# Optimization experiments

Measured on AMD Instinct MI355X. Metric: run time of the kernel, lower is better.

The kernel has to match this reference:

```python
import jax, jax.numpy as jnp
import numpy as np

N, D, NUM_CLASSES = 8192, 128, 1000


def setup_inputs() -> dict:
    key = jax.random.key(0)
    ka, kb, kt = jax.random.split(key, 3)
    fa = jax.random.normal(ka, (N, D), dtype=jnp.float32)
    fb = jax.random.normal(kb, (N, D), dtype=jnp.float32)
    # L2-normalize as in standard contrastive setups (CLIP-style)
    fa = fa / jnp.linalg.norm(fa, axis=-1, keepdims=True)
    fb = fb / jnp.linalg.norm(fb, axis=-1, keepdims=True)
    targets = jax.random.randint(kt, (N,), 0, NUM_CLASSES, dtype=jnp.int64 if jax.config.jax_enable_x64 else jnp.int32)
    T = jnp.array([100.0], dtype=jnp.float32)  # logit scale
    return {
        "T": T,
        "local_features_a": fa,
        "local_features_b": fb,
        "global_targets": targets,
        "training": 1,
    }


def reference(T, local_features_a, local_features_b, global_targets, training):
    # world_size = 1: local features ARE the global features; the chunked
    # online-softmax reduction in the original is mathematically identical
    # to a stable logsumexp over the full logits row (max is detached, so
    # gradients also match).
    eq = (global_targets[:, None] == global_targets[None, :]).astype(jnp.float32)  # [N, N] positive mask
    target_sum = jnp.sum(eq, axis=-1)  # [N]

    def one_direction(fa, fb):
        logits = T * (fa @ fb.T)  # [N, N]
        weighted = -jnp.sum(eq * logits, axis=-1)            # sum of -logits over positives
        lse = jax.nn.logsumexp(logits, axis=-1)              # online-softmax global reduction
        per_row = weighted / target_sum + lse                # [N]
        return jnp.mean(per_row)

    loss_i = one_direction(local_features_a, local_features_b)
    loss_t = one_direction(local_features_b, local_features_a)
    return (loss_i + loss_t) / 2.0
```

## Files before the change

kernel.cpp:

```cpp
#include <hip/hip_runtime.h>
#include <hip/hip_bf16.h>

#define CN 8192
#define CD 128
#define NCLS 1000
#define MAXC 256

typedef __attribute__((ext_vector_type(8))) short bf16x8;
typedef __attribute__((ext_vector_type(4))) float f32x4;

#define WS_B_OFF     0x200000u
#define WS_CNT_OFF   0x400000u
#define WS_EXTRA_OFF 0x401000u
#define WS_ROWE_OFF  0x402000u
#define WS_COLE_OFF  0x40A000u
#define WS_BKT_OFF   0x412000u
#define WS_ROWP_OFF  0x490000u
#define WS_COLP_OFF  0x890000u
#define WS_FAST_BYTES 0xA90000u
#define WS_ZERO_BYTES 0x12000u

__device__ inline unsigned short f2bf(float f) {
    unsigned int u = __float_as_uint(f);
    return (unsigned short)((u + 0x7FFFu + ((u >> 16) & 1u)) >> 16);
}

__global__ void convert_kernel(const float* __restrict__ fa, const float* __restrict__ fb,
                               unsigned short* __restrict__ Abf, unsigned short* __restrict__ Bbf,
                               const int* __restrict__ tgt,
                               int* __restrict__ cnt, unsigned short* __restrict__ bucket) {
    int gid = blockIdx.x * 256 + threadIdx.x;
    int i = gid * 4;
    const float* src = blockIdx.y == 0 ? fa : fb;
    unsigned short* dst = blockIdx.y == 0 ? Abf : Bbf;
    float4 v = *reinterpret_cast<const float4*>(src + i);
    ushort4 o;
    o.x = f2bf(v.x); o.y = f2bf(v.y); o.z = f2bf(v.z); o.w = f2bf(v.w);
    *reinterpret_cast<ushort4*>(dst + i) = o;

    if (blockIdx.y == 0 && (gid & 31) == 0) {
        int row = gid >> 5;
        int t = tgt[row];
        int slot = atomicAdd(&cnt[t], 1);
        if (slot < MAXC) bucket[t * MAXC + slot] = (unsigned short)row;
    }
}

__global__ __launch_bounds__(64) void classsum_kernel(
    const float* __restrict__ Tptr,
    const float* __restrict__ fa, const float* __restrict__ fb,
    const int* __restrict__ cnt, const unsigned short* __restrict__ bucket,
    float* __restrict__ extra) {
    const int c = blockIdx.x;
    const int lane = threadIdx.x;
    const int n = cnt[c];
    const int m = n < MAXC ? n : MAXC;
    const float* src = lane < 32 ? fa : fb;
    const int d = (lane & 31) * 4;
    float ax = 0.f, ay = 0.f, az = 0.f, aw = 0.f;
    for (int s = 0; s < m; ++s) {
        int row = bucket[c * MAXC + s];
        float4 v = *reinterpret_cast<const float4*>(src + (size_t)row * CD + d);
        ax += v.x; ay += v.y; az += v.z; aw += v.w;
    }
    float bx_ = __shfl_xor(ax, 32), by_ = __shfl_xor(ay, 32);
    float bz_ = __shfl_xor(az, 32), bw_ = __shfl_xor(aw, 32);
    float p = ax * bx_ + ay * by_ + az * bz_ + aw * bw_;
    #pragma unroll
    for (int off = 1; off < 32; off <<= 1) p += __shfl_xor(p, off);
    if (lane == 0) extra[c] = n > 0 ? (-2.0f * Tptr[0] * p / (float)n) : 0.f;
}

__global__ __launch_bounds__(256) void tile_kernel(
    const float* __restrict__ Tptr,
    const unsigned short* __restrict__ Abf,
    const unsigned short* __restrict__ Bbf,
    float* __restrict__ rowE, float* __restrict__ colE,
    float* __restrict__ rowPart, float* __restrict__ colPart,
    int store_mode)
{
    __shared__ __align__(16) unsigned short sA[128 * 128];
    __shared__ __align__(16) unsigned short sB[64 * 128];
    __shared__ float colRed[4][64];

    const int tid  = threadIdx.x;
    const int brow = blockIdx.y * 128;
    const int bcol = blockIdx.x * 64;
    const float T   = Tptr[0];
    const float Tl2 = T * 1.44269504088896340736f;

    #pragma unroll
    for (int it = 0; it < 8; ++it) {
        int idx = it * 256 + tid;
        int r = idx >> 4, q = idx & 15;
        const unsigned short* src = Abf + (size_t)(brow + r) * CD + ((q ^ (r & 7)) * 8);
        __builtin_amdgcn_global_load_lds((const __attribute__((address_space(1))) void*)src,
                                         (__attribute__((address_space(3))) void*)&sA[idx * 8],
                                         16, 0, 0);
    }
    #pragma unroll
    for (int it = 0; it < 4; ++it) {
        int idx = it * 256 + tid;
        int r = idx >> 4, q = idx & 15;
        const unsigned short* src = Bbf + (size_t)(bcol + r) * CD + ((q ^ (r & 7)) * 8);
        __builtin_amdgcn_global_load_lds((const __attribute__((address_space(1))) void*)src,
                                         (__attribute__((address_space(3))) void*)&sB[idx * 8],
                                         16, 0, 0);
    }
    __syncthreads();

    const int lane = tid & 63;
    const int w    = tid >> 6;
    const int colg = lane & 15;
    const int rowg = lane >> 4;

    f32x4 acc[2][4];
    #pragma unroll
    for (int m = 0; m < 2; ++m)
        #pragma unroll
        for (int n = 0; n < 4; ++n)
            acc[m][n] = (f32x4){0.f, 0.f, 0.f, 0.f};

    #pragma unroll
    for (int kk = 0; kk < 4; ++kk) {
        bf16x8 af[2], bfr[4];
        #pragma unroll
        for (int m = 0; m < 2; ++m) {
            int r = w * 32 + m * 16 + colg;
            int slot = (kk * 4 + rowg) ^ (r & 7);
            af[m] = *reinterpret_cast<const bf16x8*>(&sA[r * 128 + slot * 8]);
        }
        #pragma unroll
        for (int n = 0; n < 4; ++n) {
            int r = n * 16 + colg;
            int slot = (kk * 4 + rowg) ^ (r & 7);
            bfr[n] = *reinterpret_cast<const bf16x8*>(&sB[r * 128 + slot * 8]);
        }
        #pragma unroll
        for (int m = 0; m < 2; ++m)
            #pragma unroll
            for (int n = 0; n < 4; ++n)
                acc[m][n] = __builtin_amdgcn_mfma_f32_16x16x32_bf16(af[m], bfr[n], acc[m][n], 0, 0, 0);
    }

    float rE[2][4] = {{0.f}};
    float cE[4] = {0.f, 0.f, 0.f, 0.f};
    #pragma unroll
    for (int m = 0; m < 2; ++m)
        #pragma unroll
        for (int n = 0; n < 4; ++n)
            #pragma unroll
            for (int j = 0; j < 4; ++j) {
                float e = exp2f(__builtin_fmaf(acc[m][n][j], Tl2, -Tl2));
                rE[m][j] += e;
                cE[n]    += e;
            }

    #pragma unroll
    for (int m = 0; m < 2; ++m)
        #pragma unroll
        for (int j = 0; j < 4; ++j) {
            float e = rE[m][j];
            #pragma unroll
            for (int off = 1; off < 16; off <<= 1) e += __shfl_xor(e, off);
            if (colg == 0) {
                int row = brow + w * 32 + m * 16 + rowg * 4 + j;
                if (store_mode) rowPart[(size_t)blockIdx.x * CN + row] = e;
                else            atomicAdd(&rowE[row], e);
            }
        }
    #pragma unroll
    for (int n = 0; n < 4; ++n) {
        float e = cE[n];
        e += __shfl_xor(e, 16);
        e += __shfl_xor(e, 32);
        if (rowg == 0) colRed[w][n * 16 + colg] = e;
    }
    __syncthreads();
    if (tid < 64) {
        float s = colRed[0][tid] + colRed[1][tid] + colRed[2][tid] + colRed[3][tid];
        if (store_mode) colPart[(size_t)blockIdx.y * CN + bcol + tid] = s;
        else            atomicAdd(&colE[bcol + tid], s);
    }
}

__global__ __launch_bounds__(256) void finalize_kernel(
    const float* __restrict__ Tptr,
    const float* __restrict__ rowE, const float* __restrict__ colE,
    const float* __restrict__ rowPart, const float* __restrict__ colPart,
    const float* __restrict__ extra,
    float* __restrict__ out, int store_mode)
{
    __shared__ float red[4];
    const int tid = threadIdx.x;
    int i = blockIdx.x * 256 + tid;
    const float T = Tptr[0];
    float v = 0.f;
    if (i < CN) {
        float se;
        if (store_mode) {
            se = 0.f;
            #pragma unroll 4
            for (int p = 0; p < 128; ++p) se += rowPart[(size_t)p * CN + i];
        } else se = rowE[i];
        v = T + logf(se);
    } else if (i < 2 * CN) {
        int c = i - CN;
        float se;
        if (store_mode) {
            se = 0.f;
            #pragma unroll 4
            for (int p = 0; p < 64; ++p) se += colPart[(size_t)p * CN + c];
        } else se = colE[c];
        v = T + logf(se);
    } else if (i < 2 * CN + NCLS) {
        v = extra[i - 2 * CN];
    }
    #pragma unroll
    for (int off = 1; off < 64; off <<= 1) v += __shfl_xor(v, off);
    if ((tid & 63) == 0) red[tid >> 6] = v;
    __syncthreads();
    if (tid == 0) {
        float tot = red[0] + red[1] + red[2] + red[3];
        atomicAdd(out, tot * (1.0f / (2.0f * (float)CN)));
    }
}

extern "C" void kernel_launch(void* const* d_in, const int* in_sizes, int n_in,
                              void* d_out, int out_size, void* d_ws, size_t ws_size,
                              hipStream_t stream) {
    const float* T  = (const float*)d_in[0];
    const float* fa = (const float*)d_in[1];
    const float* fb = (const float*)d_in[2];
    const int* tgt  = (const int*)d_in[3];
    float* out      = (float*)d_out;

    char* ws = (char*)d_ws;
    unsigned short* Abf = (unsigned short*)ws;
    unsigned short* Bbf = (unsigned short*)(ws + WS_B_OFF);
    int*   cnt    = (int*)(ws + WS_CNT_OFF);
    float* extra  = (float*)(ws + WS_EXTRA_OFF);
    float* rowE   = (float*)(ws + WS_ROWE_OFF);
    float* colE   = (float*)(ws + WS_COLE_OFF);
    unsigned short* bucket = (unsigned short*)(ws + WS_BKT_OFF);
    float* rowPart = (float*)(ws + WS_ROWP_OFF);
    float* colPart = (float*)(ws + WS_COLP_OFF);

    const int store_mode = (ws_size >= WS_FAST_BYTES) ? 1 : 0;

    hipMemsetAsync(out, 0, sizeof(float), stream);
    hipMemsetAsync(ws + WS_CNT_OFF, 0, WS_ZERO_BYTES, stream);

    convert_kernel<<<dim3(CN * CD / (256 * 4), 2), 256, 0, stream>>>(fa, fb, Abf, Bbf, tgt, cnt, bucket);
    classsum_kernel<<<NCLS, 64, 0, stream>>>(T, fa, fb, cnt, bucket, extra);

    dim3 grid(CN / 64, CN / 128);
    tile_kernel<<<grid, 256, 0, stream>>>(T, Abf, Bbf, rowE, colE, rowPart, colPart, store_mode);

    finalize_kernel<<<(2 * CN + NCLS + 255) / 256, 256, 0, stream>>>(
        T, rowE, colE, rowPart, colPart, extra, out, store_mode);
}
```

Baseline: 144.3 us.

## Loop each tile block over 16 column tiles with double-buffered B loads

Each tile-kernel block now keeps its 128-row A tile resident in LDS and walks 16 consecutive 64-column B tiles. The next B tile is prefetched into a second LDS buffer while the current one is used, and row exp-sums stay in registers until the end. The grid shrinks from 8192 to 512 blocks, which cuts repeated A loads and launch overhead. The finalize kernel also reduces only 8 row partials instead of 128. The trade-off is fewer concurrent blocks per CU and a barrier on every column tile.

```diff
diff --git a/kernel.cpp b/kernel.cpp
--- a/kernel.cpp
+++ b/kernel.cpp
@@ -80,12 +80,14 @@
     int store_mode)
 {
     __shared__ __align__(16) unsigned short sA[128 * 128];
-    __shared__ __align__(16) unsigned short sB[64 * 128];
-    __shared__ float colRed[4][64];
-
-    const int tid  = threadIdx.x;
-    const int brow = blockIdx.y * 128;
-    const int bcol = blockIdx.x * 64;
+    __shared__ __align__(16) unsigned short sB[2][64 * 128];
+    __shared__ float colRed[2][4][64];
+
+    const int tid   = threadIdx.x;
+    const int bx    = blockIdx.x;
+    const int by    = blockIdx.y;
+    const int brow  = by * 128;
+    const int cbase = bx * 1024;
     const float T   = Tptr[0];
     const float Tl2 = T * 1.44269504088896340736f;
 
@@ -102,9 +104,9 @@
     for (int it = 0; it < 4; ++it) {
         int idx = it * 256 + tid;
         int r = idx >> 4, q = idx & 15;
-        const unsigned short* src = Bbf + (size_t)(bcol + r) * CD + ((q ^ (r & 7)) * 8);
+        const unsigned short* src = Bbf + (size_t)(cbase + r) * CD + ((q ^ (r & 7)) * 8);
         __builtin_amdgcn_global_load_lds((const __attribute__((address_space(1))) void*)src,
-                                         (__attribute__((address_space(3))) void*)&sB[idx * 8],
+                                         (__attribute__((address_space(3))) void*)&sB[0][idx * 8],
                                          16, 0, 0);
     }
     __syncthreads();
@@ -114,47 +116,80 @@
     const int colg = lane & 15;
     const int rowg = lane >> 4;
 
-    f32x4 acc[2][4];
-    #pragma unroll
-    for (int m = 0; m < 2; ++m)
-        #pragma unroll
-        for (int n = 0; n < 4; ++n)
-            acc[m][n] = (f32x4){0.f, 0.f, 0.f, 0.f};
-
-    #pragma unroll
-    for (int kk = 0; kk < 4; ++kk) {
-        bf16x8 af[2], bfr[4];
-        #pragma unroll
-        for (int m = 0; m < 2; ++m) {
-            int r = w * 32 + m * 16 + colg;
-            int slot = (kk * 4 + rowg) ^ (r & 7);
-            af[m] = *reinterpret_cast<const bf16x8*>(&sA[r * 128 + slot * 8]);
-        }
+    float rE[2][4] = {{0.f, 0.f, 0.f, 0.f}, {0.f, 0.f, 0.f, 0.f}};
+
+    for (int ct = 0; ct < 16; ++ct) {
+        const int cur = ct & 1;
+        if (ct < 15) {
+            int bcolN = cbase + (ct + 1) * 64;
+            #pragma unroll
+            for (int it = 0; it < 4; ++it) {
+                int idx = it * 256 + tid;
+                int r = idx >> 4, q = idx & 15;
+                const unsigned short* src = Bbf + (size_t)(bcolN + r) * CD + ((q ^ (r & 7)) * 8);
+                __builtin_amdgcn_global_load_lds((const __attribute__((address_space(1))) void*)src,
+                                                 (__attribute__((address_space(3))) void*)&sB[cur ^ 1][idx * 8],
+                                                 16, 0, 0);
+            }
+        }
+
+        f32x4 acc[2][4];
+        #pragma unroll
+        for (int m = 0; m < 2; ++m)
+            #pragma unroll
+            for (int n = 0; n < 4; ++n)
+                acc[m][n] = (f32x4){0.f, 0.f, 0.f, 0.f};
+
+        #pragma unroll
+        for (int kk = 0; kk < 4; ++kk) {
+            bf16x8 af[2], bfr[4];
+            #pragma unroll
+            for (int m = 0; m < 2; ++m) {
+                int r = w * 32 + m * 16 + colg;
+                int slot = (kk * 4 + rowg) ^ (r & 7);
+                af[m] = *reinterpret_cast<const bf16x8*>(&sA[r * 128 + slot * 8]);
+            }
+            #pragma unroll
+            for (int n = 0; n < 4; ++n) {
+                int r = n * 16 + colg;
+                int slot = (kk * 4 + rowg) ^ (r & 7);
+                bfr[n] = *reinterpret_cast<const bf16x8*>(&sB[cur][r * 128 + slot * 8]);
+            }
+            #pragma unroll
+            for (int m = 0; m < 2; ++m)
+                #pragma unroll
+                for (int n = 0; n < 4; ++n)
+                    acc[m][n] = __builtin_amdgcn_mfma_f32_16x16x32_bf16(af[m], bfr[n], acc[m][n], 0, 0, 0);
+        }
+
+        float cE[4] = {0.f, 0.f, 0.f, 0.f};
+        #pragma unroll
+        for (int m = 0; m < 2; ++m)
+            #pragma unroll
+            for (int n = 0; n < 4; ++n)
+                #pragma unroll
+                for (int j = 0; j < 4; ++j) {
+                    float e = exp2f(__builtin_fmaf(acc[m][n][j], Tl2, -Tl2));
+                    rE[m][j] += e;
+                    cE[n]    += e;
+                }
+
         #pragma unroll
         for (int n = 0; n < 4; ++n) {
-            int r = n * 16 + colg;
-            int slot = (kk * 4 + rowg) ^ (r & 7);
-            bfr[n] = *reinterpret_cast<const bf16x8*>(&sB[r * 128 + slot * 8]);
-        }
-        #pragma unroll
-        for (int m = 0; m < 2; ++m)
-            #pragma unroll
-            for (int n = 0; n < 4; ++n)
-                acc[m][n] = __builtin_amdgcn_mfma_f32_16x16x32_bf16(af[m], bfr[n], acc[m][n], 0, 0, 0);
-    }
-
-    float rE[2][4] = {{0.f}};
-    float cE[4] = {0.f, 0.f, 0.f, 0.f};
-    #pragma unroll
-    for (int m = 0; m < 2; ++m)
-        #pragma unroll
-        for (int n = 0; n < 4; ++n)
-            #pragma unroll
-            for (int j = 0; j < 4; ++j) {
-                float e = exp2f(__builtin_fmaf(acc[m][n][j], Tl2, -Tl2));
-                rE[m][j] += e;
-                cE[n]    += e;
-            }
+            float e = cE[n];
+            e += __shfl_xor(e, 16);
+            e += __shfl_xor(e, 32);
+            if (rowg == 0) colRed[cur][w][n * 16 + colg] = e;
+        }
+        __syncthreads();
+        if (tid < 64) {
+            float s = colRed[cur][0][tid] + colRed[cur][1][tid]
+                    + colRed[cur][2][tid] + colRed[cur][3][tid];
+            int col = cbase + ct * 64 + tid;
+            if (store_mode) colPart[(size_t)by * CN + col] = s;
+            else            atomicAdd(&colE[col], s);
+        }
+    }
 
     #pragma unroll
     for (int m = 0; m < 2; ++m)
@@ -165,23 +200,10 @@
             for (int off = 1; off < 16; off <<= 1) e += __shfl_xor(e, off);
             if (colg == 0) {
                 int row = brow + w * 32 + m * 16 + rowg * 4 + j;
-                if (store_mode) rowPart[(size_t)blockIdx.x * CN + row] = e;
+                if (store_mode) rowPart[(size_t)bx * CN + row] = e;
                 else            atomicAdd(&rowE[row], e);
             }
         }
-    #pragma unroll
-    for (int n = 0; n < 4; ++n) {
-        float e = cE[n];
-        e += __shfl_xor(e, 16);
-        e += __shfl_xor(e, 32);
-        if (rowg == 0) colRed[w][n * 16 + colg] = e;
-    }
-    __syncthreads();
-    if (tid < 64) {
-        float s = colRed[0][tid] + colRed[1][tid] + colRed[2][tid] + colRed[3][tid];
-        if (store_mode) colPart[(size_t)blockIdx.y * CN + bcol + tid] = s;
-        else            atomicAdd(&colE[bcol + tid], s);
-    }
 }
 
 __global__ __launch_bounds__(256) void finalize_kernel(
@@ -200,8 +222,8 @@
         float se;
         if (store_mode) {
             se = 0.f;
-            #pragma unroll 4
-            for (int p = 0; p < 128; ++p) se += rowPart[(size_t)p * CN + i];
+            #pragma unroll
+            for (int p = 0; p < 8; ++p) se += rowPart[(size_t)p * CN + i];
         } else se = rowE[i];
         v = T + logf(se);
     } else if (i < 2 * CN) {
@@ -254,7 +276,7 @@
     convert_kernel<<<dim3(CN * CD / (256 * 4), 2), 256, 0, stream>>>(fa, fb, Abf, Bbf, tgt, cnt, bucket);
     classsum_kernel<<<NCLS, 64, 0, stream>>>(T, fa, fb, cnt, bucket, extra);
 
-    dim3 grid(CN / 64, CN / 128);
+    dim3 grid(8, 64);
     tile_kernel<<<grid, 256, 0, stream>>>(T, Abf, Bbf, rowE, colE, rowPart, colPart, store_mode);
 
     finalize_kernel<<<(2 * CN + NCLS + 255) / 256, 256, 0, stream>>>(
```

Result: faster. 131.4 us (-8.9%).
